# Kernel optimization log

Measured on AMD Instinct MI355X. Metric: run time of the kernel, lower is better.

## Reference

```python
import jax, jax.numpy as jnp
import numpy as np

# Forest-Ruth symplectic coefficients
THETA = 1.0 / (2.0 - 2.0 ** (1.0 / 3.0))
C1 = THETA / 2.0
C2 = (1.0 - THETA) / 2.0
C3 = (1.0 - THETA) / 2.0
C4 = THETA / 2.0
D1 = THETA
D2 = 1.0 - 2.0 * THETA
D3 = THETA
DT = 0.01          # self.dt
DT_SCALE = 1.0
PI = np.float32(np.pi)


def _wrap_torus(x):
    # topology_id == 1: wrap coordinates onto the torus [-pi, pi)
    return (x + PI) % (2.0 * PI) - PI


def setup_inputs() -> dict:
    key = jax.random.key(0)
    k0, k1, k2, k3, k4 = jax.random.split(key, 5)
    B, D, K = 32768, 512, 64
    x = jax.random.normal(k0, (B, D), jnp.float32)
    v = jax.random.normal(k1, (B, D), jnp.float32)
    force = 0.1 * jax.random.normal(k2, (B, D), jnp.float32)
    U = 0.05 * jax.random.normal(k3, (D, K), jnp.float32)  # low-rank Christoffel factor
    W = 0.05 * jax.random.normal(k4, (K, D), jnp.float32)
    return {"x": x, "v": v, "force": force, "U": U, "W": W, "steps": 4}


def reference(x, v, force, U, W, steps):
    dt = DT * DT_SCALE

    def acceleration(tx, tv):
        # Christoffel contraction Gamma^i_{jk} v^j v^k with low-rank Gamma = U (.)^2 W
        h = tv @ U                 # [B, K]
        christ = (h * h) @ W       # [B, D]
        return -christ + force     # a = -Gamma(v,v) + external force

    cx, cv = x, v
    for _ in range(steps):
        x1 = _wrap_torus(cx + C1 * dt * cv)
        v1 = cv + D1 * dt * acceleration(x1, cv)
        x2 = _wrap_torus(x1 + C2 * dt * v1)
        v2 = v1 + D2 * dt * acceleration(x2, v1)
        x3 = _wrap_torus(x2 + C3 * dt * v2)
        v3 = v2 + D3 * dt * acceleration(x3, v2)
        cx, cv = _wrap_torus(x3 + C4 * dt * v3), v3
    return (cx, cv)
```

## Files before the change

### kernel.cpp

```cpp
#include <hip/hip_runtime.h>


#define NTH 512

#define VF0 0
#define VF1 8192
#define GF0 16384
#define GF1 17408
#define HB  18432
#define FB  20608
#define LDS_WORDS 37120
#define LDS_BYTES (LDS_WORDS*4)

typedef __attribute__((ext_vector_type(8))) short short8;
typedef __attribute__((ext_vector_type(16))) float float16;

__device__ __forceinline__ float wrap_torus(float y) {
    const float PI_F  = 3.14159265358979323846f;
    const float TPI_F = 6.28318530717958647692f;
    float t = y + PI_F;
    if (t >= TPI_F) t -= TPI_F;
    else if (t < 0.0f) t += TPI_F;
    return t - PI_F;
}

__device__ __forceinline__ void split2(float v, unsigned short& hi, unsigned short& lo) {
    unsigned u = __float_as_uint(v);
    unsigned h = (u + 0x7fffu + ((u >> 16) & 1u)) >> 16;
    hi = (unsigned short)h;
    float hf = __uint_as_float(h << 16);
    float r = v - hf;
    unsigned u2 = __float_as_uint(r);
    unsigned l = (u2 + 0x7fffu + ((u2 >> 16) & 1u)) >> 16;
    lo = (unsigned short)l;
}

__device__ __forceinline__ unsigned pack_split(float v) {
    unsigned short hi, lo;
    split2(v, hi, lo);
    return (((unsigned)hi) << 16) | (unsigned)lo;
}

__device__ __forceinline__ void unpack_frag(uint4 l4, uint4 h4, short8& fhi, short8& flo) {
    fhi[0]=(short)(l4.x>>16); flo[0]=(short)(l4.x&0xffffu);
    fhi[1]=(short)(l4.y>>16); flo[1]=(short)(l4.y&0xffffu);
    fhi[2]=(short)(l4.z>>16); flo[2]=(short)(l4.z&0xffffu);
    fhi[3]=(short)(l4.w>>16); flo[3]=(short)(l4.w&0xffffu);
    fhi[4]=(short)(h4.x>>16); flo[4]=(short)(h4.x&0xffffu);
    fhi[5]=(short)(h4.y>>16); flo[5]=(short)(h4.y&0xffffu);
    fhi[6]=(short)(h4.z>>16); flo[6]=(short)(h4.z&0xffffu);
    fhi[7]=(short)(h4.w>>16); flo[7]=(short)(h4.w&0xffffu);
}

__global__ void fr_prep(const float* __restrict__ Um, const float* __restrict__ Wm,
                        unsigned short* __restrict__ usw, unsigned short* __restrict__ wsw) {
    int tid = blockIdx.x * 256 + threadIdx.x;
    int lane = tid & 63;
    if (tid < 4096) {
        int c   = (tid >> 6) & 7;
        int ks4 = (tid >> 9) & 3;
        int nt1 = (tid >> 11) & 1;
        int fbase = (((nt1 * 4 + ks4) * 8 + c) * 2) * 512;
        #pragma unroll
        for (int j = 0; j < 8; ++j) {
            int d = 128 * ks4 + 16 * c + 8 * (lane >> 5) + j;
            int n = 32 * nt1 + (lane & 31);
            unsigned short hi, lo;
            split2(Um[d * 64 + n], hi, lo);
            usw[fbase + lane * 8 + j] = hi;
            usw[fbase + 512 + lane * 8 + j] = lo;
        }
    } else {
        int id = tid - 4096;
        lane = id & 63;
        int kk = (id >> 6) & 3;
        int nt = (id >> 8) & 15;
        int fbase = ((nt * 4 + kk) * 2) * 512;
        #pragma unroll
        for (int j = 0; j < 8; ++j) {
            int k = 16 * kk + 8 * (lane >> 5) + j;
            int n = 32 * nt + (lane & 31);
            unsigned short hi, lo;
            split2(Wm[k * 512 + n], hi, lo);
            wsw[fbase + lane * 8 + j] = hi;
            wsw[fbase + 512 + lane * 8 + j] = lo;
        }
    }
}

__global__ __launch_bounds__(NTH, 2) void fr_mfma(
    const float* __restrict__ xin, const float* __restrict__ vin,
    const float* __restrict__ fin,
    const short8* __restrict__ usw, const short8* __restrict__ wsw,
    float* __restrict__ xout, float* __restrict__ vout)
{
    extern __shared__ float lds[];
    unsigned int* ldsu = (unsigned int*)lds;

    const int t = threadIdx.x;
    const int lane = t & 63;
    const int w = __builtin_amdgcn_readfirstlane(t >> 6);
    const int nt1 = w & 1;
    const int ks4 = w >> 1;
    const int rhalf = lane >> 5;
    const int R0 = (int)blockIdx.x * 32;

    const double theta = 1.0 / (2.0 - 1.2599210498948732);
    const float c1dt = (float)(theta * 0.5 * 0.01);
    const float c2dt = (float)((1.0 - theta) * 0.5 * 0.01);
    const float d1dt = (float)(theta * 0.01);
    const float d2dt = (float)((1.0 - 2.0 * theta) * 0.01);

    short8 Uhi[8], Ulo[8], Whi[2][4], Wlo[2][4];
    {
        int ub = ((nt1 * 4 + ks4) * 8) * 2;
        #pragma unroll
        for (int c = 0; c < 8; ++c) {
            Uhi[c] = usw[(ub + 2 * c + 0) * 64 + lane];
            Ulo[c] = usw[(ub + 2 * c + 1) * 64 + lane];
        }
        #pragma unroll
        for (int nt = 0; nt < 2; ++nt) {
            int wb = ((w * 2 + nt) * 4) * 2;
            #pragma unroll
            for (int kk = 0; kk < 4; ++kk) {
                Whi[nt][kk] = wsw[(wb + 2 * kk + 0) * 64 + lane];
                Wlo[nt][kk] = wsw[(wb + 2 * kk + 1) * 64 + lane];
            }
        }
    }

    float vst[2][16], xst[2][16];
    int cg[2];
    cg[0] = (w * 2 + 0) * 32 + (lane & 31);
    cg[1] = (w * 2 + 1) * 32 + (lane & 31);
    #pragma unroll
    for (int nt = 0; nt < 2; ++nt) {
        #pragma unroll
        for (int r = 0; r < 16; ++r) {
            int rrow = (r & 3) + 8 * (r >> 2) + 4 * rhalf;
            size_t idx = (size_t)(R0 + rrow) * 512 + cg[nt];
            vst[nt][r] = vin[idx];
            xst[nt][r] = xin[idx];
        }
    }

    {
        #pragma unroll
        for (int it = 0; it < 8; ++it) {
            int flat = it * 2048 + t * 4;
            float4 val = *(const float4*)(fin + (size_t)R0 * 512 + flat);
            int row = flat >> 9, col = flat & 511;
            *(float4*)(lds + FB + row * 516 + col) = val;
        }
    }

    #pragma unroll
    for (int nt = 0; nt < 2; ++nt)
        #pragma unroll
        for (int r = 0; r < 16; ++r)
            xst[nt][r] = wrap_torus(xst[nt][r] + c1dt * vst[nt][r]);

    #pragma unroll
    for (int nt = 0; nt < 2; ++nt) {
        #pragma unroll
        for (int r = 0; r < 16; ++r) {
            int m = (r & 3) + 8 * (r >> 2) + 4 * rhalf;
            int d = cg[nt];
            unsigned p = pack_split(vst[nt][r]);
            int kst = d >> 4, lb = (d >> 3) & 1, j = d & 7;
            ldsu[((j >> 2) ? VF1 : VF0) + (kst * 64 + m + 32 * lb) * 4 + (j & 3)] = p;
        }
    }
    for (int i = t; i < 32 * 68; i += NTH) lds[HB + i] = 0.0f;

    #pragma unroll 1
    for (int sub = 0; sub < 12; ++sub) {
        const int idx3 = sub - (sub / 3) * 3;
        const float ddt = (idx3 == 1) ? d2dt : d1dt;
        const float xc  = (idx3 == 2) ? c1dt : c2dt;
        const bool dbl  = (idx3 == 2) && (sub != 11);

        __syncthreads();

        float16 acc0, acc1;
        #pragma unroll
        for (int i = 0; i < 16; ++i) { acc0[i] = 0.0f; acc1[i] = 0.0f; }
        #pragma unroll
        for (int c = 0; c < 8; ++c) {
            int kst = ks4 * 8 + c;
            uint4 pl = *(const uint4*)&ldsu[VF0 + (kst * 64 + lane) * 4];
            uint4 ph = *(const uint4*)&ldsu[VF1 + (kst * 64 + lane) * 4];
            short8 Ahi, Alo;
            unpack_frag(pl, ph, Ahi, Alo);
            acc0 = __builtin_amdgcn_mfma_f32_32x32x16_bf16(Ahi, Uhi[c], acc0, 0, 0, 0);
            acc1 = __builtin_amdgcn_mfma_f32_32x32x16_bf16(Alo, Uhi[c], acc1, 0, 0, 0);
            acc1 = __builtin_amdgcn_mfma_f32_32x32x16_bf16(Ahi, Ulo[c], acc1, 0, 0, 0);
        }
        {
            int kcol = nt1 * 32 + (lane & 31);
            #pragma unroll
            for (int r = 0; r < 16; ++r) {
                int m = (r & 3) + 8 * (r >> 2) + 4 * rhalf;
                atomicAdd(&lds[HB + m * 68 + kcol], acc0[r] + acc1[r]);
            }
        }
        __syncthreads();

        {
            int grow = t >> 4;
            int k4 = (t & 15) * 4;
            float4 h4 = *(const float4*)&lds[HB + grow * 68 + k4];
            uint4 gp;
            gp.x = pack_split(h4.x * h4.x);
            gp.y = pack_split(h4.y * h4.y);
            gp.z = pack_split(h4.z * h4.z);
            gp.w = pack_split(h4.w * h4.w);
            int kst2 = k4 >> 4, lb2 = (k4 >> 3) & 1, jb = k4 & 7;
            *(uint4*)&ldsu[((jb >> 2) ? GF1 : GF0) + (kst2 * 64 + grow + 32 * lb2) * 4] = gp;
        }
        __syncthreads();

        float16 cA, cB;
        #pragma unroll
        for (int i = 0; i < 16; ++i) { cA[i] = 0.0f; cB[i] = 0.0f; }
        #pragma unroll
        for (int kk = 0; kk < 4; ++kk) {
            uint4 pl = *(const uint4*)&ldsu[GF0 + (kk * 64 + lane) * 4];
            uint4 ph = *(const uint4*)&ldsu[GF1 + (kk * 64 + lane) * 4];
            short8 Ahi, Alo;
            unpack_frag(pl, ph, Ahi, Alo);
            cA = __builtin_amdgcn_mfma_f32_32x32x16_bf16(Ahi, Whi[0][kk], cA, 0, 0, 0);
            cB = __builtin_amdgcn_mfma_f32_32x32x16_bf16(Ahi, Whi[1][kk], cB, 0, 0, 0);
            cA = __builtin_amdgcn_mfma_f32_32x32x16_bf16(Alo, Whi[0][kk], cA, 0, 0, 0);
            cB = __builtin_amdgcn_mfma_f32_32x32x16_bf16(Alo, Whi[1][kk], cB, 0, 0, 0);
            cA = __builtin_amdgcn_mfma_f32_32x32x16_bf16(Ahi, Wlo[0][kk], cA, 0, 0, 0);
            cB = __builtin_amdgcn_mfma_f32_32x32x16_bf16(Ahi, Wlo[1][kk], cB, 0, 0, 0);
        }

        #pragma unroll
        for (int nt = 0; nt < 2; ++nt) {
            #pragma unroll
            for (int r = 0; r < 16; ++r) {
                int m = (r & 3) + 8 * (r >> 2) + 4 * rhalf;
                float fv = lds[FB + m * 516 + cg[nt]];
                float christ = (nt == 0) ? cA[r] : cB[r];
                float vn = vst[nt][r] + ddt * (fv - christ);
                vst[nt][r] = vn;
                float xn = wrap_torus(xst[nt][r] + xc * vn);
                if (dbl) xn = wrap_torus(xn + c1dt * vn);
                xst[nt][r] = xn;
            }
        }

        if (sub != 11) {
            #pragma unroll
            for (int nt = 0; nt < 2; ++nt) {
                #pragma unroll
                for (int r = 0; r < 16; ++r) {
                    int m = (r & 3) + 8 * (r >> 2) + 4 * rhalf;
                    int d = cg[nt];
                    unsigned p = pack_split(vst[nt][r]);
                    int kst = d >> 4, lb = (d >> 3) & 1, j = d & 7;
                    ldsu[((j >> 2) ? VF1 : VF0) + (kst * 64 + m + 32 * lb) * 4 + (j & 3)] = p;
                }
            }
            for (int i = t; i < 32 * 68; i += NTH) lds[HB + i] = 0.0f;
        }
    }

    #pragma unroll
    for (int nt = 0; nt < 2; ++nt) {
        #pragma unroll
        for (int r = 0; r < 16; ++r) {
            int rrow = (r & 3) + 8 * (r >> 2) + 4 * rhalf;
            size_t idx = (size_t)(R0 + rrow) * 512 + cg[nt];
            xout[idx] = xst[nt][r];
            vout[idx] = vst[nt][r];
        }
    }
}

extern "C" void kernel_launch(void* const* d_in, const int* in_sizes, int n_in,
                              void* d_out, int out_size, void* d_ws, size_t ws_size,
                              hipStream_t stream) {
    const float* x = (const float*)d_in[0];
    const float* v = (const float*)d_in[1];
    const float* f = (const float*)d_in[2];
    const float* U = (const float*)d_in[3];
    const float* W = (const float*)d_in[4];

    float* xout = (float*)d_out;
    float* vout = xout + (size_t)32768 * 512;

    unsigned short* usw = (unsigned short*)d_ws;
    unsigned short* wsw = usw + 65536;

    fr_prep<<<32, 256, 0, stream>>>(U, W, usw, wsw);

    hipFuncSetAttribute(reinterpret_cast<const void*>(fr_mfma),
                        hipFuncAttributeMaxDynamicSharedMemorySize, LDS_BYTES);
    fr_mfma<<<1024, NTH, LDS_BYTES, stream>>>(
        x, v, f, (const short8*)usw, (const short8*)wsw, xout, vout);
}
```

Measured before the change: 1.224 ms.

## Replace block barrier with per-group LDS flags, swizzle fragments, move x to LDS

Replaces the top-of-substep __syncthreads with per-ks4 group flag counters in LDS, so each pair of waves proceeds once its own producers have written their velocity fragments. Also XOR-swizzles the velocity and Christoffel fragment layouts to cut LDS bank conflicts, and software-pipelines the fragment loads. It keeps force in registers and moves x into LDS, and zeros the H buffer right where it is read. The spin-wait adds sleep and atomic overhead, and the flag counting across substeps is subtle and could be racy.

```diff
diff --git a/kernel.cpp b/kernel.cpp
--- a/kernel.cpp
+++ b/kernel.cpp
@@ -8,8 +8,9 @@
 #define GF0 16384
 #define GF1 17408
 #define HB  18432
-#define FB  20608
-#define LDS_WORDS 37120
+#define XB  20608
+#define FLAGS 36992
+#define LDS_WORDS 36996
 #define LDS_BYTES (LDS_WORDS*4)
 
 typedef __attribute__((ext_vector_type(8))) short short8;
@@ -52,6 +53,12 @@
     fhi[7]=(short)(h4.w>>16); flo[7]=(short)(h4.w&0xffffu);
 }
 
+__device__ __forceinline__ void vf_store(unsigned int* ldsu, int m, int d, unsigned p) {
+    int kst = d >> 4, lb = (d >> 3) & 1, j = d & 7;
+    int slot = (m + 32 * lb) ^ ((kst & 7) << 2);
+    ldsu[((j >> 2) ? VF1 : VF0) + (kst * 64 + slot) * 4 + (j & 3)] = p;
+}
+
 __global__ void fr_prep(const float* __restrict__ Um, const float* __restrict__ Wm,
                         unsigned short* __restrict__ usw, unsigned short* __restrict__ wsw) {
     int tid = blockIdx.x * 256 + threadIdx.x;
@@ -96,6 +103,7 @@
 {
     extern __shared__ float lds[];
     unsigned int* ldsu = (unsigned int*)lds;
+    unsigned int* flagp = &ldsu[FLAGS];
 
     const int t = threadIdx.x;
     const int lane = t & 63;
@@ -130,7 +138,7 @@
         }
     }
 
-    float vst[2][16], xst[2][16];
+    float vst[2][16], fst[2][16];
     int cg[2];
     cg[0] = (w * 2 + 0) * 32 + (lane & 31);
     cg[1] = (w * 2 + 1) * 32 + (lane & 31);
@@ -138,41 +146,22 @@
     for (int nt = 0; nt < 2; ++nt) {
         #pragma unroll
         for (int r = 0; r < 16; ++r) {
-            int rrow = (r & 3) + 8 * (r >> 2) + 4 * rhalf;
-            size_t idx = (size_t)(R0 + rrow) * 512 + cg[nt];
-            vst[nt][r] = vin[idx];
-            xst[nt][r] = xin[idx];
-        }
-    }
-
-    {
-        #pragma unroll
-        for (int it = 0; it < 8; ++it) {
-            int flat = it * 2048 + t * 4;
-            float4 val = *(const float4*)(fin + (size_t)R0 * 512 + flat);
-            int row = flat >> 9, col = flat & 511;
-            *(float4*)(lds + FB + row * 516 + col) = val;
-        }
-    }
-
-    #pragma unroll
-    for (int nt = 0; nt < 2; ++nt)
-        #pragma unroll
-        for (int r = 0; r < 16; ++r)
-            xst[nt][r] = wrap_torus(xst[nt][r] + c1dt * vst[nt][r]);
-
-    #pragma unroll
-    for (int nt = 0; nt < 2; ++nt) {
-        #pragma unroll
-        for (int r = 0; r < 16; ++r) {
             int m = (r & 3) + 8 * (r >> 2) + 4 * rhalf;
-            int d = cg[nt];
-            unsigned p = pack_split(vst[nt][r]);
-            int kst = d >> 4, lb = (d >> 3) & 1, j = d & 7;
-            ldsu[((j >> 2) ? VF1 : VF0) + (kst * 64 + m + 32 * lb) * 4 + (j & 3)] = p;
-        }
-    }
+            size_t idx = (size_t)(R0 + m) * 512 + cg[nt];
+            float vv = vin[idx];
+            float xv = xin[idx];
+            vst[nt][r] = vv;
+            fst[nt][r] = fin[idx];
+            lds[XB + m * 512 + cg[nt]] = wrap_torus(xv + c1dt * vv);
+            vf_store(ldsu, m, cg[nt], pack_split(vv));
+        }
+    }
+
     for (int i = t; i < 32 * 68; i += NTH) lds[HB + i] = 0.0f;
+    if (t < 4) flagp[t] = 0u;
+    __syncthreads();
+
+    unsigned int* myflag = &flagp[ks4];
 
     #pragma unroll 1
     for (int sub = 0; sub < 12; ++sub) {
@@ -181,18 +170,33 @@
         const float xc  = (idx3 == 2) ? c1dt : c2dt;
         const bool dbl  = (idx3 == 2) && (sub != 11);
 
-        __syncthreads();
+        if (sub > 0) {
+            unsigned target = 2u * (unsigned)sub;
+            while (__hip_atomic_load(myflag, __ATOMIC_ACQUIRE,
+                                     __HIP_MEMORY_SCOPE_WORKGROUP) < target)
+                __builtin_amdgcn_s_sleep(1);
+        }
 
         float16 acc0, acc1;
         #pragma unroll
         for (int i = 0; i < 16; ++i) { acc0[i] = 0.0f; acc1[i] = 0.0f; }
+        uint4 pl, ph;
+        {
+            int kst = ks4 * 8;
+            pl = *(const uint4*)&ldsu[VF0 + (kst * 64 + lane) * 4];
+            ph = *(const uint4*)&ldsu[VF1 + (kst * 64 + lane) * 4];
+        }
         #pragma unroll
         for (int c = 0; c < 8; ++c) {
-            int kst = ks4 * 8 + c;
-            uint4 pl = *(const uint4*)&ldsu[VF0 + (kst * 64 + lane) * 4];
-            uint4 ph = *(const uint4*)&ldsu[VF1 + (kst * 64 + lane) * 4];
+            uint4 cpl = pl, cph = ph;
+            if (c < 7) {
+                int kst = ks4 * 8 + c + 1;
+                int slot = lane ^ (((c + 1) & 7) << 2);
+                pl = *(const uint4*)&ldsu[VF0 + (kst * 64 + slot) * 4];
+                ph = *(const uint4*)&ldsu[VF1 + (kst * 64 + slot) * 4];
+            }
             short8 Ahi, Alo;
-            unpack_frag(pl, ph, Ahi, Alo);
+            unpack_frag(cpl, cph, Ahi, Alo);
             acc0 = __builtin_amdgcn_mfma_f32_32x32x16_bf16(Ahi, Uhi[c], acc0, 0, 0, 0);
             acc1 = __builtin_amdgcn_mfma_f32_32x32x16_bf16(Alo, Uhi[c], acc1, 0, 0, 0);
             acc1 = __builtin_amdgcn_mfma_f32_32x32x16_bf16(Ahi, Ulo[c], acc1, 0, 0, 0);
@@ -211,25 +215,35 @@
             int grow = t >> 4;
             int k4 = (t & 15) * 4;
             float4 h4 = *(const float4*)&lds[HB + grow * 68 + k4];
+            float4 z4; z4.x = 0.0f; z4.y = 0.0f; z4.z = 0.0f; z4.w = 0.0f;
+            *(float4*)&lds[HB + grow * 68 + k4] = z4;
             uint4 gp;
             gp.x = pack_split(h4.x * h4.x);
             gp.y = pack_split(h4.y * h4.y);
             gp.z = pack_split(h4.z * h4.z);
             gp.w = pack_split(h4.w * h4.w);
             int kst2 = k4 >> 4, lb2 = (k4 >> 3) & 1, jb = k4 & 7;
-            *(uint4*)&ldsu[((jb >> 2) ? GF1 : GF0) + (kst2 * 64 + grow + 32 * lb2) * 4] = gp;
+            int slot2 = (grow + 32 * lb2) ^ ((kst2 & 7) << 2);
+            *(uint4*)&ldsu[((jb >> 2) ? GF1 : GF0) + (kst2 * 64 + slot2) * 4] = gp;
         }
         __syncthreads();
 
         float16 cA, cB;
         #pragma unroll
         for (int i = 0; i < 16; ++i) { cA[i] = 0.0f; cB[i] = 0.0f; }
+        uint4 gl, gh;
+        gl = *(const uint4*)&ldsu[GF0 + (0 * 64 + lane) * 4];
+        gh = *(const uint4*)&ldsu[GF1 + (0 * 64 + lane) * 4];
         #pragma unroll
         for (int kk = 0; kk < 4; ++kk) {
-            uint4 pl = *(const uint4*)&ldsu[GF0 + (kk * 64 + lane) * 4];
-            uint4 ph = *(const uint4*)&ldsu[GF1 + (kk * 64 + lane) * 4];
+            uint4 cgl = gl, cgh = gh;
+            if (kk < 3) {
+                int slot = lane ^ (((kk + 1) & 7) << 2);
+                gl = *(const uint4*)&ldsu[GF0 + ((kk + 1) * 64 + slot) * 4];
+                gh = *(const uint4*)&ldsu[GF1 + ((kk + 1) * 64 + slot) * 4];
+            }
             short8 Ahi, Alo;
-            unpack_frag(pl, ph, Ahi, Alo);
+            unpack_frag(cgl, cgh, Ahi, Alo);
             cA = __builtin_amdgcn_mfma_f32_32x32x16_bf16(Ahi, Whi[0][kk], cA, 0, 0, 0);
             cB = __builtin_amdgcn_mfma_f32_32x32x16_bf16(Ahi, Whi[1][kk], cB, 0, 0, 0);
             cA = __builtin_amdgcn_mfma_f32_32x32x16_bf16(Alo, Whi[0][kk], cA, 0, 0, 0);
@@ -243,29 +257,22 @@
             #pragma unroll
             for (int r = 0; r < 16; ++r) {
                 int m = (r & 3) + 8 * (r >> 2) + 4 * rhalf;
-                float fv = lds[FB + m * 516 + cg[nt]];
                 float christ = (nt == 0) ? cA[r] : cB[r];
-                float vn = vst[nt][r] + ddt * (fv - christ);
+                float vn = vst[nt][r] + ddt * (fst[nt][r] - christ);
                 vst[nt][r] = vn;
-                float xn = wrap_torus(xst[nt][r] + xc * vn);
+                int xw = XB + m * 512 + cg[nt];
+                float xo = lds[xw];
+                float xn = wrap_torus(xo + xc * vn);
                 if (dbl) xn = wrap_torus(xn + c1dt * vn);
-                xst[nt][r] = xn;
+                lds[xw] = xn;
+                if (sub != 11) vf_store(ldsu, m, cg[nt], pack_split(vn));
             }
         }
 
         if (sub != 11) {
-            #pragma unroll
-            for (int nt = 0; nt < 2; ++nt) {
-                #pragma unroll
-                for (int r = 0; r < 16; ++r) {
-                    int m = (r & 3) + 8 * (r >> 2) + 4 * rhalf;
-                    int d = cg[nt];
-                    unsigned p = pack_split(vst[nt][r]);
-                    int kst = d >> 4, lb = (d >> 3) & 1, j = d & 7;
-                    ldsu[((j >> 2) ? VF1 : VF0) + (kst * 64 + m + 32 * lb) * 4 + (j & 3)] = p;
-                }
-            }
-            for (int i = t; i < 32 * 68; i += NTH) lds[HB + i] = 0.0f;
+            if (lane == 0)
+                __hip_atomic_fetch_add(myflag, 1u, __ATOMIC_RELEASE,
+                                       __HIP_MEMORY_SCOPE_WORKGROUP);
         }
     }
 
@@ -273,9 +280,9 @@
     for (int nt = 0; nt < 2; ++nt) {
         #pragma unroll
         for (int r = 0; r < 16; ++r) {
-            int rrow = (r & 3) + 8 * (r >> 2) + 4 * rhalf;
-            size_t idx = (size_t)(R0 + rrow) * 512 + cg[nt];
-            xout[idx] = xst[nt][r];
+            int m = (r & 3) + 8 * (r >> 2) + 4 * rhalf;
+            size_t idx = (size_t)(R0 + m) * 512 + cg[nt];
+            xout[idx] = lds[XB + m * 512 + cg[nt]];
             vout[idx] = vst[nt][r];
         }
     }
```

Result: slower. 1.675 ms (+36.8%).
